# Performance work log

Measured on AMD Instinct MI355X. Metric: run time of the kernel, lower is better.

The kernel has to match this reference:

```python
import jax, jax.numpy as jnp
import numpy as np

B, C, ROWS, COLS = 16, 1, 128, 128
E, H, L, VOCAB = 64, 32, 3, 258


def setup_inputs() -> dict:
    key = jax.random.key(0)
    ks = jax.random.split(key, 18)
    s = 0.05
    d = {
        "x": jax.random.randint(ks[0], (B, C, ROWS, COLS), 0, VOCAB, dtype=jnp.int32),
        "embed_table": jax.random.normal(ks[1], (VOCAB, E), jnp.float32) * s,
    }
    in_sizes = [E + 1, H, H]
    k = 2
    for l in range(L):
        d[f"w_ih_l{l}"] = jax.random.normal(ks[k], (3 * H, in_sizes[l]), jnp.float32) * s; k += 1
        d[f"w_hh_l{l}"] = jax.random.normal(ks[k], (3 * H, H), jnp.float32) * s; k += 1
        d[f"b_ih_l{l}"] = jax.random.normal(ks[k], (3 * H,), jnp.float32) * s; k += 1
        d[f"b_hh_l{l}"] = jax.random.normal(ks[k], (3 * H,), jnp.float32) * s; k += 1
    d["w_h2e"] = jax.random.normal(ks[14], (E + 1, H), jnp.float32) * s
    d["b_h2e"] = jax.random.normal(ks[15], (E + 1,), jnp.float32) * s
    d["w_out"] = jax.random.normal(ks[16], (VOCAB, H), jnp.float32) * s
    d["b_out"] = jax.random.normal(ks[17], (VOCAB,), jnp.float32) * s
    return d


def _forward(x, embed_table, wih, whh, bih, bhh, w_h2e, b_h2e, w_out, b_out):
    b, c, rows, cols = x.shape
    T = cols * c  # GRU sequence length per row
    Hh = whh[0].shape[1]
    nL = len(wih)

    xf = x.reshape(b, rows, T)
    emb = embed_table[xf]  # [B, rows, T, E]
    # normalized row coordinate in [-1, 1), appended as extra feature
    row_pos = jnp.arange(rows, dtype=emb.dtype) / rows * 2.0 - 1.0
    row_feat = jnp.broadcast_to(row_pos[None, :, None, None], (b, rows, T, 1))
    xin = jnp.concatenate([emb, row_feat], axis=-1)  # [B, rows, T, E+1]

    def gru_step(h, x_t):
        # h: [L, B, H]; x_t: [B, E+1]. torch GRU gate order: r, z, n.
        inp = x_t
        hs = []
        for l in range(nL):
            gi = inp @ wih[l].T + bih[l]
            gh = h[l] @ whh[l].T + bhh[l]
            ir, iz, inn = jnp.split(gi, 3, axis=-1)
            hr, hz, hn = jnp.split(gh, 3, axis=-1)
            r = jax.nn.sigmoid(ir + hr)
            z = jax.nn.sigmoid(iz + hz)
            n = jnp.tanh(inn + r * hn)
            hl = (1.0 - z) * n + z * h[l]
            hs.append(hl)
            inp = hl
        return jnp.stack(hs), inp  # emit top-layer output

    def row_step(prev_out, x_row):
        # prev_out: [B, T, H] top-layer GRU output of previous row
        comb = x_row + prev_out @ w_h2e.T + b_h2e  # [B, T, E+1]
        h0 = jnp.zeros((nL, b, Hh), comb.dtype)  # fresh h0 per row, as in torch
        _, out = jax.lax.scan(gru_step, h0, jnp.swapaxes(comb, 0, 1))  # [T, B, H]
        out = jnp.swapaxes(out, 0, 1)  # [B, T, H]
        return out, out

    prev0 = jnp.zeros((b, T, Hh), xin.dtype)
    _, outs = jax.lax.scan(row_step, prev0, jnp.swapaxes(xin, 0, 1))  # [rows, B, T, H]
    outs = jnp.swapaxes(outs, 0, 1)  # [B, rows, T, H]
    pred = outs @ w_out.T + b_out  # [B, rows, T, 258]
    return pred.reshape(b, c, rows, cols, VOCAB)


def reference(x, embed_table, w_ih_l0, w_hh_l0, b_ih_l0, b_hh_l0,
              w_ih_l1, w_hh_l1, b_ih_l1, b_hh_l1,
              w_ih_l2, w_hh_l2, b_ih_l2, b_hh_l2,
              w_h2e, b_h2e, w_out, b_out):
    return _forward(x, embed_table,
                    (w_ih_l0, w_ih_l1, w_ih_l2),
                    (w_hh_l0, w_hh_l1, w_hh_l2),
                    (b_ih_l0, b_ih_l1, b_ih_l2),
                    (b_hh_l0, b_hh_l1, b_hh_l2),
                    w_h2e, b_h2e, w_out, b_out)
```

## Files before the change

kernel.cpp:

```cpp
#include <hip/hip_runtime.h>
#include <math.h>

#define BATCH 16
#define RWS   128
#define TT    128
#define HH    32
#define GG    96
#define NBG   2
#define BPG   8
#define WSTR  34
#define FSTR  16

#define H2_BYTES   (BATCH*RWS*TT*HH*4)
#define FLAG_OFF   H2_BYTES
#define FLAG_BYTES (RWS*NBG*FSTR*4)
#define PTAB_OFF   (FLAG_OFF + FLAG_BYTES)
#define WF_OFF     (PTAB_OFF + 258*GG*4)

__device__ __forceinline__ float sigm(float x) { return 1.0f / (1.0f + __expf(-x)); }
__device__ __forceinline__ float tanhfast(float x) {
  x = fminf(fmaxf(x, -15.0f), 15.0f);
  float e = __expf(2.0f * x);
  return (e - 1.0f) / (e + 1.0f);
}

__device__ __forceinline__ float dot32(const float* __restrict__ w, const float* __restrict__ v) {
  float a0 = 0.f, a1 = 0.f;
#pragma unroll
  for (int k = 0; k < HH; k += 4) {
    float2 w0 = *(const float2*)(w + k);
    float2 w1 = *(const float2*)(w + k + 2);
    float2 v0 = *(const float2*)(v + k);
    float2 v1 = *(const float2*)(v + k + 2);
    a0 = fmaf(w0.x, v0.x, fmaf(w0.y, v0.y, a0));
    a1 = fmaf(w1.x, v1.x, fmaf(w1.y, v1.y, a1));
  }
  return a0 + a1;
}

__global__ __launch_bounds__(128)
void prep_kernel(const float* __restrict__ emb, const float* __restrict__ wih0,
                 const float* __restrict__ bih0, const float* __restrict__ wh2e,
                 const float* __restrict__ bh2e, float* __restrict__ Ptab,
                 float* __restrict__ Wfo) {
  const int blk = blockIdx.x, tid = threadIdx.x;
  if (blk < 258) {
    if (tid < GG) {
      const float* wr = wih0 + tid * 65;
      const float* e  = emb + blk * 64;
      float acc = bih0[tid];
      for (int k = 0; k < 64; ++k) acc = fmaf(wr[k], e[k], acc);
      for (int k = 0; k < 65; ++k) acc = fmaf(wr[k], bh2e[k], acc);
      Ptab[blk * GG + tid] = acc;
    }
  } else {
    const int g = blk - 258;
    if (tid < HH) {
      const float* wr = wih0 + g * 65;
      float acc = 0.f;
      for (int k = 0; k < 65; ++k) acc = fmaf(wr[k], wh2e[k * HH + tid], acc);
      Wfo[g * HH + tid] = acc;
    }
  }
}

__device__ __forceinline__ void loadmat(const float* __restrict__ src, float* __restrict__ dst, int tid) {
  for (int i = tid; i < GG * HH; i += 256) dst[(i >> 5) * WSTR + (i & 31)] = src[i];
}

__global__ __launch_bounds__(256)
void rnn_kernel(const int* __restrict__ xg, const float* __restrict__ wih0,
                const float* __restrict__ whh0g, const float* __restrict__ bhh0g,
                const float* __restrict__ wih1g, const float* __restrict__ whh1g,
                const float* __restrict__ bih1g, const float* __restrict__ bhh1g,
                const float* __restrict__ wih2g, const float* __restrict__ whh2g,
                const float* __restrict__ bih2g, const float* __restrict__ bhh2g,
                const float* __restrict__ Ptab, const float* __restrict__ Wfg,
                float* __restrict__ h2buf, int* __restrict__ flags) {
  extern __shared__ float lds[];
  float* Wf    = lds;
  float* Whh0  = Wf   + GG * WSTR;
  float* Wih1  = Whh0 + GG * WSTR;
  float* Whh1  = Wih1 + GG * WSTR;
  float* Wih2  = Whh1 + GG * WSTR;
  float* Whh2  = Wih2 + GG * WSTR;
  float* bias  = Whh2 + GG * WSTR;
  float* rp    = bias + 5 * GG;
  float* prevs = rp + GG;
  float* h0s   = prevs + BPG * HH;
  float* h1s   = h0s + BPG * HH;
  float* h2s   = h1s + BPG * HH;

  const int tid = threadIdx.x;
  const int r   = blockIdx.x & (RWS - 1);
  const int bg  = blockIdx.x >> 7;
  const int j   = tid & 31;
  const int b   = tid >> 5;
  const int bglob = bg * BPG + b;

  loadmat(Wfg,   Wf,   tid);
  loadmat(whh0g, Whh0, tid);
  loadmat(wih1g, Wih1, tid);
  loadmat(whh1g, Whh1, tid);
  loadmat(wih2g, Wih2, tid);
  loadmat(whh2g, Whh2, tid);
  {
    const float rowpos = (float)r * (2.0f / 128.0f) - 1.0f;
    for (int i = tid; i < GG; i += 256) {
      bias[i]          = bhh0g[i];
      bias[GG + i]     = bih1g[i];
      bias[2 * GG + i] = bhh1g[i];
      bias[3 * GG + i] = bih2g[i];
      bias[4 * GG + i] = bhh2g[i];
      rp[i] = wih0[i * 65 + 64] * rowpos;
    }
  }
  h0s[tid] = 0.f; h1s[tid] = 0.f; h2s[tid] = 0.f; prevs[tid] = 0.f;
  __syncthreads();

  float h0r = 0.f, h1r = 0.f, h2r = 0.f;
  const size_t xbase = (size_t)(bglob * RWS + r) * TT;
  const size_t obase = (size_t)(bglob * RWS + r) * TT * HH + j;
  const size_t pbase = (r > 0) ? ((size_t)(bglob * RWS + (r - 1)) * TT * HH + j) : 0;
  int* myflag = flags + (r * NBG + bg) * FSTR;
  const int* pflag = (r > 0) ? (flags + ((r - 1) * NBG + bg) * FSTR) : flags;
  const float* hb0 = h0s + b * HH;
  const float* hb1 = h1s + b * HH;
  const float* hb2 = h2s + b * HH;
  const float* pb  = prevs + b * HH;

  int vcur = xg[xbase];

  for (int t = 0; t < TT; ++t) {
    int vnext = (t < TT - 1) ? xg[xbase + t + 1] : 0;
    float Pr = Ptab[vcur * GG + j];
    float Pz = Ptab[vcur * GG + 32 + j];
    float Pn = Ptab[vcur * GG + 64 + j];

    if (r > 0) {
      if (tid == 0) {
        const int want = t + 1;
        while (__hip_atomic_load(pflag, __ATOMIC_RELAXED, __HIP_MEMORY_SCOPE_AGENT) < want)
          __builtin_amdgcn_s_sleep(1);
      }
      __syncthreads();
    }
    float pv = 0.f;
    if (r > 0)
      pv = __hip_atomic_load(h2buf + pbase + (size_t)t * HH, __ATOMIC_RELAXED, __HIP_MEMORY_SCOPE_AGENT);

    float ghr0 = bias[j]          + dot32(Whh0 + j * WSTR, hb0);
    float ghz0 = bias[32 + j]     + dot32(Whh0 + (32 + j) * WSTR, hb0);
    float ghn0 = bias[64 + j]     + dot32(Whh0 + (64 + j) * WSTR, hb0);
    float ghr1 = bias[2*GG + j]      + dot32(Whh1 + j * WSTR, hb1);
    float ghz1 = bias[2*GG + 32 + j] + dot32(Whh1 + (32 + j) * WSTR, hb1);
    float ghn1 = bias[2*GG + 64 + j] + dot32(Whh1 + (64 + j) * WSTR, hb1);
    float ghr2 = bias[4*GG + j]      + dot32(Whh2 + j * WSTR, hb2);
    float ghz2 = bias[4*GG + 32 + j] + dot32(Whh2 + (32 + j) * WSTR, hb2);
    float ghn2 = bias[4*GG + 64 + j] + dot32(Whh2 + (64 + j) * WSTR, hb2);

    prevs[b * HH + j] = pv;
    __syncthreads();

    {
      float gir = Pr + rp[j]        + dot32(Wf + j * WSTR, pb);
      float giz = Pz + rp[32 + j]   + dot32(Wf + (32 + j) * WSTR, pb);
      float gin = Pn + rp[64 + j]   + dot32(Wf + (64 + j) * WSTR, pb);
      float rg = sigm(gir + ghr0);
      float zg = sigm(giz + ghz0);
      float ng = tanhfast(gin + rg * ghn0);
      h0r = (1.f - zg) * ng + zg * h0r;
    }
    h0s[b * HH + j] = h0r;
    __syncthreads();

    {
      float gir = bias[GG + j]        + dot32(Wih1 + j * WSTR, hb0);
      float giz = bias[GG + 32 + j]   + dot32(Wih1 + (32 + j) * WSTR, hb0);
      float gin = bias[GG + 64 + j]   + dot32(Wih1 + (64 + j) * WSTR, hb0);
      float rg = sigm(gir + ghr1);
      float zg = sigm(giz + ghz1);
      float ng = tanhfast(gin + rg * ghn1);
      h1r = (1.f - zg) * ng + zg * h1r;
    }
    h1s[b * HH + j] = h1r;
    __syncthreads();

    {
      float gir = bias[3*GG + j]        + dot32(Wih2 + j * WSTR, hb1);
      float giz = bias[3*GG + 32 + j]   + dot32(Wih2 + (32 + j) * WSTR, hb1);
      float gin = bias[3*GG + 64 + j]   + dot32(Wih2 + (64 + j) * WSTR, hb1);
      float rg = sigm(gir + ghr2);
      float zg = sigm(giz + ghz2);
      float ng = tanhfast(gin + rg * ghn2);
      h2r = (1.f - zg) * ng + zg * h2r;
    }
    h2s[b * HH + j] = h2r;
    __hip_atomic_store(h2buf + obase + (size_t)t * HH, h2r,
                       __ATOMIC_RELAXED, __HIP_MEMORY_SCOPE_AGENT);
    __syncthreads();
    if (tid == 0)
      __hip_atomic_store(myflag, t + 1, __ATOMIC_RELAXED, __HIP_MEMORY_SCOPE_AGENT);

    vcur = vnext;
  }
}

__global__ __launch_bounds__(256)
void proj_kernel(const float* __restrict__ h2buf, const float* __restrict__ wout,
                 const float* __restrict__ bout, float* __restrict__ out) {
  __shared__ float stage[32 * 258];
  const int tid = threadIdx.x;
  const int p = tid & 31, vq = tid >> 5;
  const size_t pos = (size_t)blockIdx.x * 32 + p;
  const float* hrow = h2buf + pos * HH;
  float h[HH];
#pragma unroll
  for (int k = 0; k < HH; k += 4) {
    float4 f = *(const float4*)(hrow + k);
    h[k] = f.x; h[k + 1] = f.y; h[k + 2] = f.z; h[k + 3] = f.w;
  }
#pragma unroll 1
  for (int vi = 0; vi <= 32; ++vi) {
    int v = vq + vi * 8;
    if (v < 258) {
      const float* wrow = wout + v * HH;
      float a0 = bout[v], a1 = 0.f;
#pragma unroll
      for (int k = 0; k < HH; k += 4) {
        float4 w = *(const float4*)(wrow + k);
        a0 = fmaf(w.x, h[k],     fmaf(w.y, h[k + 1], a0));
        a1 = fmaf(w.z, h[k + 2], fmaf(w.w, h[k + 3], a1));
      }
      stage[p * 258 + v] = a0 + a1;
    }
  }
  __syncthreads();
  float* o = out + (size_t)blockIdx.x * 32 * 258;
#pragma unroll 1
  for (int i = tid; i < 32 * 258; i += 256) o[i] = stage[i];
}

extern "C" void kernel_launch(void* const* d_in, const int* in_sizes, int n_in,
                              void* d_out, int out_size, void* d_ws, size_t ws_size,
                              hipStream_t stream) {
  const int*   x    = (const int*)d_in[0];
  const float* emb  = (const float*)d_in[1];
  const float* wih0 = (const float*)d_in[2];
  const float* whh0 = (const float*)d_in[3];
  const float* bih0 = (const float*)d_in[4];
  const float* bhh0 = (const float*)d_in[5];
  const float* wih1 = (const float*)d_in[6];
  const float* whh1 = (const float*)d_in[7];
  const float* bih1 = (const float*)d_in[8];
  const float* bhh1 = (const float*)d_in[9];
  const float* wih2 = (const float*)d_in[10];
  const float* whh2 = (const float*)d_in[11];
  const float* bih2 = (const float*)d_in[12];
  const float* bhh2 = (const float*)d_in[13];
  const float* wh2e = (const float*)d_in[14];
  const float* bh2e = (const float*)d_in[15];
  const float* wout = (const float*)d_in[16];
  const float* bout = (const float*)d_in[17];
  float* out = (float*)d_out;

  char*  ws    = (char*)d_ws;
  float* h2buf = (float*)ws;
  int*   flags = (int*)(ws + FLAG_OFF);
  float* Ptab  = (float*)(ws + PTAB_OFF);
  float* Wf    = (float*)(ws + WF_OFF);

  hipMemsetAsync(flags, 0, FLAG_BYTES, stream);
  prep_kernel<<<354, 128, 0, stream>>>(emb, wih0, bih0, wh2e, bh2e, Ptab, Wf);

  const int rnn_lds_bytes = (6 * GG * WSTR + 5 * GG + GG + 4 * BPG * HH) * 4;
  hipFuncSetAttribute((const void*)rnn_kernel,
                      hipFuncAttributeMaxDynamicSharedMemorySize, rnn_lds_bytes);
  rnn_kernel<<<256, 256, rnn_lds_bytes, stream>>>(
      x, wih0, whh0, bhh0, wih1, whh1, bih1, bhh1, wih2, whh2, bih2, bhh2,
      Ptab, Wf, h2buf, flags);

  proj_kernel<<<8192, 256, 0, stream>>>(h2buf, wout, bout, out);
}
```

Before: 1.811 ms.

## Pipeline eight rows per block as an intra-block wavefront, one sync per step

Each block now owns eight consecutive image rows of one batch element instead of one row across eight batch elements. Row s runs s timesteps behind row s-1 inside the block and reads the previous row's top-layer output from a double-buffered shared array. Cross-block flag handoff through global memory now happens only between groups of eight rows, and per-step barriers drop from four to one. The aim is to cut the long chain of global-memory flag waits and barrier latency on the row-to-row dependency. The cost is a longer pipeline fill and drain, and reliance on same-wavefront execution order for hidden-state reuse between layers without barriers.

```diff
diff --git a/kernel.cpp b/kernel.cpp
--- a/kernel.cpp
+++ b/kernel.cpp
@@ -6,14 +6,14 @@
 #define TT    128
 #define HH    32
 #define GG    96
-#define NBG   2
-#define BPG   8
+#define RPB   8
+#define NRG   (RWS/RPB)
 #define WSTR  34
 #define FSTR  16
 
 #define H2_BYTES   (BATCH*RWS*TT*HH*4)
 #define FLAG_OFF   H2_BYTES
-#define FLAG_BYTES (RWS*NBG*FSTR*4)
+#define FLAG_BYTES (NRG*BATCH*FSTR*4)
 #define PTAB_OFF   (FLAG_OFF + FLAG_BYTES)
 #define WF_OFF     (PTAB_OFF + 258*GG*4)
 
@@ -85,18 +85,18 @@
   float* Wih2  = Whh1 + GG * WSTR;
   float* Whh2  = Wih2 + GG * WSTR;
   float* bias  = Whh2 + GG * WSTR;
-  float* rp    = bias + 5 * GG;
-  float* prevs = rp + GG;
-  float* h0s   = prevs + BPG * HH;
-  float* h1s   = h0s + BPG * HH;
-  float* h2s   = h1s + BPG * HH;
+  float* prevs = bias + 5 * GG;
+  float* h0s   = prevs + HH;
+  float* h1s   = h0s + RPB * HH;
+  float* h2a   = h1s + RPB * HH;
+  float* h2b   = h2a + RPB * HH;
 
   const int tid = threadIdx.x;
-  const int r   = blockIdx.x & (RWS - 1);
-  const int bg  = blockIdx.x >> 7;
   const int j   = tid & 31;
-  const int b   = tid >> 5;
-  const int bglob = bg * BPG + b;
+  const int s   = tid >> 5;
+  const int g   = blockIdx.x >> 4;
+  const int bat = blockIdx.x & 15;
+  const int row = g * RPB + s;
 
   loadmat(Wfg,   Wf,   tid);
   loadmat(whh0g, Whh0, tid);
@@ -104,103 +104,117 @@
   loadmat(whh1g, Whh1, tid);
   loadmat(wih2g, Wih2, tid);
   loadmat(whh2g, Whh2, tid);
-  {
-    const float rowpos = (float)r * (2.0f / 128.0f) - 1.0f;
-    for (int i = tid; i < GG; i += 256) {
-      bias[i]          = bhh0g[i];
-      bias[GG + i]     = bih1g[i];
-      bias[2 * GG + i] = bhh1g[i];
-      bias[3 * GG + i] = bih2g[i];
-      bias[4 * GG + i] = bhh2g[i];
-      rp[i] = wih0[i * 65 + 64] * rowpos;
-    }
-  }
-  h0s[tid] = 0.f; h1s[tid] = 0.f; h2s[tid] = 0.f; prevs[tid] = 0.f;
+  for (int i = tid; i < GG; i += 256) {
+    bias[i]          = bhh0g[i];
+    bias[GG + i]     = bih1g[i];
+    bias[2 * GG + i] = bhh1g[i];
+    bias[3 * GG + i] = bih2g[i];
+    bias[4 * GG + i] = bhh2g[i];
+  }
+  h0s[tid] = 0.f; h1s[tid] = 0.f; h2a[tid] = 0.f; h2b[tid] = 0.f;
+  if (tid < HH) prevs[tid] = 0.f;
+
+  const float rowpos = (float)row * (2.0f / 128.0f) - 1.0f;
+  const float rpr = wih0[j * 65 + 64] * rowpos;
+  const float rpz = wih0[(32 + j) * 65 + 64] * rowpos;
+  const float rpn = wih0[(64 + j) * 65 + 64] * rowpos;
   __syncthreads();
 
   float h0r = 0.f, h1r = 0.f, h2r = 0.f;
-  const size_t xbase = (size_t)(bglob * RWS + r) * TT;
-  const size_t obase = (size_t)(bglob * RWS + r) * TT * HH + j;
-  const size_t pbase = (r > 0) ? ((size_t)(bglob * RWS + (r - 1)) * TT * HH + j) : 0;
-  int* myflag = flags + (r * NBG + bg) * FSTR;
-  const int* pflag = (r > 0) ? (flags + ((r - 1) * NBG + bg) * FSTR) : flags;
-  const float* hb0 = h0s + b * HH;
-  const float* hb1 = h1s + b * HH;
-  const float* hb2 = h2s + b * HH;
-  const float* pb  = prevs + b * HH;
+  const size_t xbase = (size_t)(bat * RWS + row) * TT;
+  const size_t obase = (size_t)(bat * RWS + row) * TT * HH + j;
+  const size_t pbase = (row > 0) ? ((size_t)(bat * RWS + (row - 1)) * TT * HH + j) : 0;
+  int* myflag = flags + (g * BATCH + bat) * FSTR;
+  const int* pflag = flags + ((g > 0 ? g - 1 : 0) * BATCH + bat) * FSTR;
+  const float* hb0 = h0s + s * HH;
+  const float* hb1 = h1s + s * HH;
 
   int vcur = xg[xbase];
 
-  for (int t = 0; t < TT; ++t) {
-    int vnext = (t < TT - 1) ? xg[xbase + t + 1] : 0;
-    float Pr = Ptab[vcur * GG + j];
-    float Pz = Ptab[vcur * GG + 32 + j];
-    float Pn = Ptab[vcur * GG + 64 + j];
-
-    if (r > 0) {
+  for (int i = 0; i < TT + RPB - 1; ++i) {
+    const int t = i - s;
+    const bool act = (t >= 0) && (t < TT);
+    const float* h2rd = (i & 1) ? h2a : h2b;
+    float*       h2w  = (i & 1) ? h2b : h2a;
+
+    const int tn = t + 1;
+    const int vnext = (tn >= 0 && tn < TT) ? xg[xbase + tn] : 0;
+    const float Pr = Ptab[vcur * GG + j];
+    const float Pz = Ptab[vcur * GG + 32 + j];
+    const float Pn = Ptab[vcur * GG + 64 + j];
+
+    if (g > 0 && i < TT) {
       if (tid == 0) {
-        const int want = t + 1;
+        const int want = i + 1;
         while (__hip_atomic_load(pflag, __ATOMIC_RELAXED, __HIP_MEMORY_SCOPE_AGENT) < want)
           __builtin_amdgcn_s_sleep(1);
       }
-      __syncthreads();
-    }
-    float pv = 0.f;
-    if (r > 0)
-      pv = __hip_atomic_load(h2buf + pbase + (size_t)t * HH, __ATOMIC_RELAXED, __HIP_MEMORY_SCOPE_AGENT);
-
-    float ghr0 = bias[j]          + dot32(Whh0 + j * WSTR, hb0);
-    float ghz0 = bias[32 + j]     + dot32(Whh0 + (32 + j) * WSTR, hb0);
-    float ghn0 = bias[64 + j]     + dot32(Whh0 + (64 + j) * WSTR, hb0);
-    float ghr1 = bias[2*GG + j]      + dot32(Whh1 + j * WSTR, hb1);
-    float ghz1 = bias[2*GG + 32 + j] + dot32(Whh1 + (32 + j) * WSTR, hb1);
-    float ghn1 = bias[2*GG + 64 + j] + dot32(Whh1 + (64 + j) * WSTR, hb1);
-    float ghr2 = bias[4*GG + j]      + dot32(Whh2 + j * WSTR, hb2);
-    float ghz2 = bias[4*GG + 32 + j] + dot32(Whh2 + (32 + j) * WSTR, hb2);
-    float ghn2 = bias[4*GG + 64 + j] + dot32(Whh2 + (64 + j) * WSTR, hb2);
-
-    prevs[b * HH + j] = pv;
+    }
     __syncthreads();
 
-    {
-      float gir = Pr + rp[j]        + dot32(Wf + j * WSTR, pb);
-      float giz = Pz + rp[32 + j]   + dot32(Wf + (32 + j) * WSTR, pb);
-      float gin = Pn + rp[64 + j]   + dot32(Wf + (64 + j) * WSTR, pb);
-      float rg = sigm(gir + ghr0);
-      float zg = sigm(giz + ghz0);
-      float ng = tanhfast(gin + rg * ghn0);
-      h0r = (1.f - zg) * ng + zg * h0r;
-    }
-    h0s[b * HH + j] = h0r;
-    __syncthreads();
-
-    {
-      float gir = bias[GG + j]        + dot32(Wih1 + j * WSTR, hb0);
-      float giz = bias[GG + 32 + j]   + dot32(Wih1 + (32 + j) * WSTR, hb0);
-      float gin = bias[GG + 64 + j]   + dot32(Wih1 + (64 + j) * WSTR, hb0);
-      float rg = sigm(gir + ghr1);
-      float zg = sigm(giz + ghz1);
-      float ng = tanhfast(gin + rg * ghn1);
-      h1r = (1.f - zg) * ng + zg * h1r;
-    }
-    h1s[b * HH + j] = h1r;
-    __syncthreads();
-
-    {
-      float gir = bias[3*GG + j]        + dot32(Wih2 + j * WSTR, hb1);
-      float giz = bias[3*GG + 32 + j]   + dot32(Wih2 + (32 + j) * WSTR, hb1);
-      float gin = bias[3*GG + 64 + j]   + dot32(Wih2 + (64 + j) * WSTR, hb1);
-      float rg = sigm(gir + ghr2);
-      float zg = sigm(giz + ghz2);
-      float ng = tanhfast(gin + rg * ghn2);
-      h2r = (1.f - zg) * ng + zg * h2r;
-    }
-    h2s[b * HH + j] = h2r;
-    __hip_atomic_store(h2buf + obase + (size_t)t * HH, h2r,
-                       __ATOMIC_RELAXED, __HIP_MEMORY_SCOPE_AGENT);
-    __syncthreads();
-    if (tid == 0)
-      __hip_atomic_store(myflag, t + 1, __ATOMIC_RELAXED, __HIP_MEMORY_SCOPE_AGENT);
+    if (s == 0 && g > 0 && act) {
+      prevs[j] = __hip_atomic_load(h2buf + pbase + (size_t)t * HH,
+                                   __ATOMIC_RELAXED, __HIP_MEMORY_SCOPE_AGENT);
+    }
+
+    if (act) {
+      const float* hb2 = h2rd + s * HH;
+      float ghr0 = bias[j]          + dot32(Whh0 + j * WSTR, hb0);
+      float ghz0 = bias[32 + j]     + dot32(Whh0 + (32 + j) * WSTR, hb0);
+      float ghn0 = bias[64 + j]     + dot32(Whh0 + (64 + j) * WSTR, hb0);
+      float ghr1 = bias[2*GG + j]      + dot32(Whh1 + j * WSTR, hb1);
+      float ghz1 = bias[2*GG + 32 + j] + dot32(Whh1 + (32 + j) * WSTR, hb1);
+      float ghn1 = bias[2*GG + 64 + j] + dot32(Whh1 + (64 + j) * WSTR, hb1);
+      float ghr2 = bias[4*GG + j]      + dot32(Whh2 + j * WSTR, hb2);
+      float ghz2 = bias[4*GG + 32 + j] + dot32(Whh2 + (32 + j) * WSTR, hb2);
+      float ghn2 = bias[4*GG + 64 + j] + dot32(Whh2 + (64 + j) * WSTR, hb2);
+
+      const float* pb = (s == 0) ? prevs : (h2rd + (s - 1) * HH);
+      {
+        float gir = Pr + rpr + dot32(Wf + j * WSTR, pb);
+        float giz = Pz + rpz + dot32(Wf + (32 + j) * WSTR, pb);
+        float gin = Pn + rpn + dot32(Wf + (64 + j) * WSTR, pb);
+        float rg = sigm(gir + ghr0);
+        float zg = sigm(giz + ghz0);
+        float ng = tanhfast(gin + rg * ghn0);
+        h0r = (1.f - zg) * ng + zg * h0r;
+      }
+      h0s[s * HH + j] = h0r;
+
+      {
+        float gir = bias[GG + j]        + dot32(Wih1 + j * WSTR, hb0);
+        float giz = bias[GG + 32 + j]   + dot32(Wih1 + (32 + j) * WSTR, hb0);
+        float gin = bias[GG + 64 + j]   + dot32(Wih1 + (64 + j) * WSTR, hb0);
+        float rg = sigm(gir + ghr1);
+        float zg = sigm(giz + ghz1);
+        float ng = tanhfast(gin + rg * ghn1);
+        h1r = (1.f - zg) * ng + zg * h1r;
+      }
+      h1s[s * HH + j] = h1r;
+
+      {
+        float gir = bias[3*GG + j]        + dot32(Wih2 + j * WSTR, hb1);
+        float giz = bias[3*GG + 32 + j]   + dot32(Wih2 + (32 + j) * WSTR, hb1);
+        float gin = bias[3*GG + 64 + j]   + dot32(Wih2 + (64 + j) * WSTR, hb1);
+        float rg = sigm(gir + ghr2);
+        float zg = sigm(giz + ghz2);
+        float ng = tanhfast(gin + rg * ghn2);
+        h2r = (1.f - zg) * ng + zg * h2r;
+      }
+      h2w[s * HH + j] = h2r;
+
+      if (s == RPB - 1) {
+        __hip_atomic_store(h2buf + obase + (size_t)t * HH, h2r,
+                           __ATOMIC_RELAXED, __HIP_MEMORY_SCOPE_AGENT);
+      } else {
+        h2buf[obase + (size_t)t * HH] = h2r;
+      }
+    }
+
+    if (tid == 224 && i >= RPB - 1) {
+      asm volatile("s_waitcnt vmcnt(0)" ::: "memory");
+      __hip_atomic_store(myflag, i - (RPB - 2), __ATOMIC_RELAXED, __HIP_MEMORY_SCOPE_AGENT);
+    }
 
     vcur = vnext;
   }
@@ -273,10 +287,10 @@
   hipMemsetAsync(flags, 0, FLAG_BYTES, stream);
   prep_kernel<<<354, 128, 0, stream>>>(emb, wih0, bih0, wh2e, bh2e, Ptab, Wf);
 
-  const int rnn_lds_bytes = (6 * GG * WSTR + 5 * GG + GG + 4 * BPG * HH) * 4;
+  const int rnn_lds_bytes = (6 * GG * WSTR + 5 * GG + HH + 4 * RPB * HH) * 4;
   hipFuncSetAttribute((const void*)rnn_kernel,
                       hipFuncAttributeMaxDynamicSharedMemorySize, rnn_lds_bytes);
-  rnn_kernel<<<256, 256, rnn_lds_bytes, stream>>>(
+  rnn_kernel<<<NRG * BATCH, 256, rnn_lds_bytes, stream>>>(
       x, wih0, whh0, bhh0, wih1, whh1, bih1, bhh1, wih2, whh2, bih2, bhh2,
       Ptab, Wf, h2buf, flags);
 
```

After: 1.830 ms. About the same (+1.1%).
